# Performance work log

Hardware: AMD Instinct MI355X
Metric: run time of the kernel (lower is better)

The kernel has to match this reference:

```python
import jax, jax.numpy as jnp
import numpy as np

# Multi-scale deformable attention encoder (Mask2Former pixel decoder transformer)
SHAPES = ((64, 64), (32, 32), (16, 16))  # (H, W) per level, strides 8/16/32 of 512x512
HEADS, POINTS, DM = 8, 4, 256
HD = DM // HEADS
NLVL = len(SHAPES)
NLAYERS = 6
STARTS = np.concatenate([[0], np.cumsum([h * w for h, w in SHAPES])])


def layer_norm(x, g, b, eps=1e-5):
    m = x.mean(-1, keepdims=True)
    v = ((x - m) ** 2).mean(-1, keepdims=True)
    return (x - m) * jax.lax.rsqrt(v + eps) * g + b


def ref_points(B, dtype):
    # valid_ratios == 1 (masks are all-False in the module)
    pts = []
    for H, W in SHAPES:
        ys = (jnp.arange(H, dtype=dtype) + 0.5) / H
        xs = (jnp.arange(W, dtype=dtype) + 0.5) / W
        gy, gx = jnp.meshgrid(ys, xs, indexing='ij')
        pts.append(jnp.stack([gx.reshape(-1), gy.reshape(-1)], -1))
    ref = jnp.concatenate(pts, 0)  # [Q,2]
    return jnp.broadcast_to(ref[None, :, None, :], (B, ref.shape[0], NLVL, 2))


def bilinear(value, loc, H, W):
    # grid_sample(align_corners=False, padding_mode='zeros')
    # value: [B,heads,H*W,d]; loc: [B,Q,heads,P,2] normalized to [0,1]
    x = loc[..., 0] * W - 0.5
    y = loc[..., 1] * H - 0.5
    x0f = jnp.floor(x); y0f = jnp.floor(y)
    lx = x - x0f; ly = y - y0f
    x0 = x0f.astype(jnp.int32); y0 = y0f.astype(jnp.int32)
    out = 0.
    for dx, dy, w in ((0, 0, (1 - lx) * (1 - ly)), (1, 0, lx * (1 - ly)),
                      (0, 1, (1 - lx) * ly), (1, 1, lx * ly)):
        xi = x0 + dx; yi = y0 + dy
        valid = (xi >= 0) & (xi < W) & (yi >= 0) & (yi < H)
        idx = jnp.clip(yi, 0, H - 1) * W + jnp.clip(xi, 0, W - 1)  # [B,Q,heads,P]
        idx_t = jnp.transpose(idx, (0, 2, 1, 3))  # [B,heads,Q,P]
        Bq, hq, Qq, Pq = idx_t.shape
        g = jnp.take_along_axis(value, idx_t.reshape(Bq, hq, Qq * Pq, 1), axis=2)
        g = g.reshape(Bq, hq, Qq, Pq, HD)
        wv = (w * valid).transpose(0, 2, 1, 3)[..., None]  # [B,heads,Q,P,1]
        out = out + g * wv
    return out  # [B,heads,Q,P,d]


def msda(query, src, ref, p):
    off_w, off_b, aw_w, aw_b, val_w, val_b, out_w, out_b = p
    B, Q, _ = query.shape
    value = (src @ val_w.T + val_b).reshape(B, Q, HEADS, HD).transpose(0, 2, 1, 3)  # [B,h,Q,d]
    off = (query @ off_w.T + off_b).reshape(B, Q, HEADS, NLVL, POINTS, 2)
    aw = (query @ aw_w.T + aw_b).reshape(B, Q, HEADS, NLVL * POINTS)
    aw = jax.nn.softmax(aw, -1).reshape(B, Q, HEADS, NLVL, POINTS)
    norm = jnp.array([[W, H] for H, W in SHAPES], dtype=query.dtype)  # [L,2] as (W,H)
    loc = ref[:, :, None, :, None, :] + off / norm[None, None, None, :, None, :]
    samp = []
    for l, (H, W) in enumerate(SHAPES):
        v = value[:, :, STARTS[l]:STARTS[l + 1], :]
        samp.append(bilinear(v, loc[:, :, :, l], H, W))  # [B,h,Q,P,d]
    samp = jnp.stack(samp, 3)  # [B,h,Q,L,P,d]
    w = aw.transpose(0, 2, 1, 3, 4)[..., None]  # [B,h,Q,L,P,1]
    o = (samp * w).sum((3, 4)).transpose(0, 2, 1, 3).reshape(B, Q, DM)
    return o @ out_w.T + out_b


def reference(src0, src1, src2, pos0, pos1, pos2, level_embed,
              off_w, off_b, aw_w, aw_b, val_w, val_b, out_w, out_b,
              ln1_g, ln1_b, ffn1_w, ffn1_b, ffn2_w, ffn2_b, ln2_g, ln2_b):
    srcs, poss = [src0, src1, src2], [pos0, pos1, pos2]
    B = src0.shape[0]
    xs, ps = [], []
    for l, (s, pe) in enumerate(zip(srcs, poss)):
        b, c, h, w = s.shape
        xs.append(s.reshape(b, c, h * w).transpose(0, 2, 1))
        ps.append(pe.reshape(b, c, h * w).transpose(0, 2, 1) + level_embed[l])
    x = jnp.concatenate(xs, 1)    # [B,Q,C]
    pos = jnp.concatenate(ps, 1)  # [B,Q,C]
    ref = ref_points(B, x.dtype)
    for i in range(NLAYERS):
        q = x + pos
        attn = msda(q, x, ref, (off_w[i], off_b[i], aw_w[i], aw_b[i],
                                val_w[i], val_b[i], out_w[i], out_b[i]))
        x = layer_norm(x + attn, ln1_g[i], ln1_b[i])
        h = jax.nn.relu(x @ ffn1_w[i].T + ffn1_b[i])
        x = layer_norm(x + h @ ffn2_w[i].T + ffn2_b[i], ln2_g[i], ln2_b[i])
    return x  # memory [B,Q,C]


def setup_inputs() -> dict:
    key = jax.random.key(0)
    ks = jax.random.split(key, 16)
    s = 0.02
    inp = {}
    inp['src0'] = jax.random.normal(ks[0], (4, 256, 64, 64), jnp.float32)
    inp['src1'] = jax.random.normal(ks[1], (4, 256, 32, 32), jnp.float32)
    inp['src2'] = jax.random.normal(ks[2], (4, 256, 16, 16), jnp.float32)
    inp['pos0'] = jax.random.normal(ks[3], (4, 256, 64, 64), jnp.float32)
    inp['pos1'] = jax.random.normal(ks[4], (4, 256, 32, 32), jnp.float32)
    inp['pos2'] = jax.random.normal(ks[5], (4, 256, 16, 16), jnp.float32)
    inp['level_embed'] = jax.random.normal(ks[6], (3, 256), jnp.float32)
    inp['off_w'] = jax.random.normal(ks[7], (6, 192, 256), jnp.float32) * s
    inp['off_b'] = jnp.zeros((6, 192), jnp.float32)
    inp['aw_w'] = jax.random.normal(ks[8], (6, 96, 256), jnp.float32) * s
    inp['aw_b'] = jnp.zeros((6, 96), jnp.float32)
    inp['val_w'] = jax.random.normal(ks[9], (6, 256, 256), jnp.float32) * s
    inp['val_b'] = jnp.zeros((6, 256), jnp.float32)
    inp['out_w'] = jax.random.normal(ks[10], (6, 256, 256), jnp.float32) * s
    inp['out_b'] = jnp.zeros((6, 256), jnp.float32)
    inp['ln1_g'] = jnp.ones((6, 256), jnp.float32)
    inp['ln1_b'] = jnp.zeros((6, 256), jnp.float32)
    inp['ffn1_w'] = jax.random.normal(ks[11], (6, 1024, 256), jnp.float32) * s
    inp['ffn1_b'] = jnp.zeros((6, 1024), jnp.float32)
    inp['ffn2_w'] = jax.random.normal(ks[12], (6, 256, 1024), jnp.float32) * s
    inp['ffn2_b'] = jnp.zeros((6, 256), jnp.float32)
    inp['ln2_g'] = jnp.ones((6, 256), jnp.float32)
    inp['ln2_b'] = jnp.zeros((6, 256), jnp.float32)
    return inp
```

## Files before the change

kernel.cpp:

```cpp
#include <hip/hip_runtime.h>
#include <hip/hip_bf16.h>
#include <math.h>

#define BB 4
#define QTOT 5376
#define DMM 256
#define NHEADS 8
#define HDIM 32
#define NPTS 4
#define NLVLS 3
#define BQ (BB*QTOT)
#define NOA 288

typedef short bf16x8 __attribute__((ext_vector_type(8)));
typedef unsigned short u16x8 __attribute__((ext_vector_type(8)));
typedef float f32x4  __attribute__((ext_vector_type(4)));

__device__ __forceinline__ unsigned short f2b(float f) {
  unsigned int u = __float_as_uint(f);
  unsigned int r = (u + 0x7FFFu + ((u >> 16) & 1u)) >> 16;
  return (unsigned short)r;
}
__device__ __forceinline__ float b2f(unsigned short u) {
  return __uint_as_float(((unsigned int)u) << 16);
}
__device__ __forceinline__ ushort4 f2b4(float4 v) {
  ushort4 o; o.x = f2b(v.x); o.y = f2b(v.y); o.z = f2b(v.z); o.w = f2b(v.w);
  return o;
}

__device__ __forceinline__ void gload16(const void* g, void* l) {
  __builtin_amdgcn_global_load_lds(
      (const __attribute__((address_space(1))) void*)g,
      (__attribute__((address_space(3))) void*)l, 16, 0, 0);
}

__global__ __launch_bounds__(256) void transpose2(
    const float* __restrict__ src, const float* __restrict__ pos,
    const float* __restrict__ emb, float* __restrict__ x,
    unsigned short* __restrict__ pos16, int HW, int qstart)
{
  __shared__ float ts[32][33];
  __shared__ float tp[32][33];
  int hw0 = blockIdx.x * 32, c0 = blockIdx.y * 32, b = blockIdx.z;
  int tx = threadIdx.x, ty = threadIdx.y;
  const float* s = src + ((size_t)b * DMM + c0) * HW + hw0;
  const float* p = pos + ((size_t)b * DMM + c0) * HW + hw0;
#pragma unroll
  for (int j = 0; j < 4; j++) {
    ts[ty * 4 + j][tx] = s[(size_t)(ty * 4 + j) * HW + tx];
    tp[ty * 4 + j][tx] = p[(size_t)(ty * 4 + j) * HW + tx];
  }
  __syncthreads();
  float e = emb[c0 + tx];
  size_t base = ((size_t)b * QTOT + qstart + hw0) * DMM + c0;
#pragma unroll
  for (int j = 0; j < 4; j++) {
    x[base + (size_t)(ty * 4 + j) * DMM + tx] = ts[tx][ty * 4 + j];
    pos16[base + (size_t)(ty * 4 + j) * DMM + tx] = f2b(tp[tx][ty * 4 + j] + e);
  }
}

__global__ __launch_bounds__(256) void conv_b(
    const float* __restrict__ s, unsigned short* __restrict__ d, int n4)
{
  int i = blockIdx.x * 256 + threadIdx.x;
  if (i >= n4) return;
  ((ushort4*)d)[i] = f2b4(((const float4*)s)[i]);
}

__global__ __launch_bounds__(256) void pack_oa(
    const float* __restrict__ offw, const float* __restrict__ aww,
    unsigned short* __restrict__ dst)
{
  int i = blockIdx.x * 256 + threadIdx.x;
  if (i >= 6 * NOA * 64) return;
  int c4 = i & 63;
  int row = (i >> 6) % NOA;
  int l = i / (NOA * 64);
  const float* src = (row < 192)
      ? offw + ((size_t)l * 192 + row) * 256
      : aww  + ((size_t)l * 96 + (row - 192)) * 256;
  float4 v = ((const float4*)src)[c4];
  ((ushort4*)dst)[i] = f2b4(v);
}

__global__ __launch_bounds__(256) void pack_oa_bias(
    const float* __restrict__ offb, const float* __restrict__ awb,
    float* __restrict__ dst)
{
  int i = blockIdx.x * 256 + threadIdx.x;
  if (i >= 6 * NOA) return;
  int row = i % NOA, l = i / NOA;
  dst[i] = (row < 192) ? offb[l * 192 + row] : awb[l * 96 + (row - 192)];
}

__global__ __launch_bounds__(256) void prep(
    const float* __restrict__ x, const unsigned short* __restrict__ pos16,
    unsigned short* __restrict__ xb, unsigned short* __restrict__ qb, int n4)
{
  int i = blockIdx.x * 256 + threadIdx.x;
  if (i >= n4) return;
  float4 a = ((const float4*)x)[i];
  ushort4 p = ((const ushort4*)pos16)[i];
  ((ushort4*)xb)[i] = f2b4(a);
  ushort4 q;
  q.x = f2b(a.x + b2f(p.x)); q.y = f2b(a.y + b2f(p.y));
  q.z = f2b(a.z + b2f(p.z)); q.w = f2b(a.w + b2f(p.w));
  ((ushort4*)qb)[i] = q;
}

__device__ __forceinline__ void gemm_tile_body(
    const unsigned short* __restrict__ A, const unsigned short* __restrict__ W,
    int m0, int n0, int K,
    unsigned short (*As)[32], unsigned short (*Ws)[32], f32x4 acc[4][4])
{
  int tid = threadIdx.x;
  int wave = tid >> 6, lane = tid & 63;
  int lr = lane & 15;
  int lkr = ((lane >> 4) ^ (lane & 3)) * 8;
  int wrr = (wave >> 1) * 64;
  int wcc = (wave & 1) * 64;

  int srow = lane >> 2;
  int schunk = ((lane & 3) ^ (srow & 3)) * 8;
  const unsigned short* Ag = A + (size_t)(m0 + wave * 32 + srow) * K + schunk;
  const unsigned short* Wg = W + (size_t)(n0 + wave * 32 + srow) * K + schunk;

#define STAGE_BF(k0, buf)                                                      \
  { int bo = (buf) * 128 + wave * 32;                                          \
    gload16(Ag + (k0), &As[bo][0]);                                            \
    gload16(Ag + (size_t)16 * K + (k0), &As[bo + 16][0]);                      \
    gload16(Wg + (k0), &Ws[bo][0]);                                            \
    gload16(Wg + (size_t)16 * K + (k0), &Ws[bo + 16][0]); }

  STAGE_BF(0, 0);
  __syncthreads();
  int cur = 0;
  for (int k0 = 0; k0 < K; k0 += 32) {
    if (k0 + 32 < K) STAGE_BF(k0 + 32, cur ^ 1);
    int bo = cur * 128;
    bf16x8 af[4], bfv[4];
#pragma unroll
    for (int m = 0; m < 4; m++)
      af[m] = *(const bf16x8*)&As[bo + wrr + m * 16 + lr][lkr];
#pragma unroll
    for (int n = 0; n < 4; n++)
      bfv[n] = *(const bf16x8*)&Ws[bo + wcc + n * 16 + lr][lkr];
#pragma unroll
    for (int m = 0; m < 4; m++)
#pragma unroll
      for (int n = 0; n < 4; n++)
        acc[m][n] = __builtin_amdgcn_mfma_f32_16x16x32_bf16(af[m], bfv[n], acc[m][n], 0, 0, 0);
    __syncthreads();
    cur ^= 1;
  }
#undef STAGE_BF
}

__device__ __forceinline__ void gemm_epilogue(
    const float* __restrict__ bias, void* __restrict__ Cout,
    int m0, int n0, int N, int relu, int bfout, f32x4 acc[4][4])
{
  int tid = threadIdx.x;
  int wave = tid >> 6, lane = tid & 63;
  int lr = lane & 15;
  int wrr = (wave >> 1) * 64;
  int wcc = (wave & 1) * 64;
  float* C32 = (float*)Cout;
  unsigned short* C16 = (unsigned short*)Cout;
#pragma unroll
  for (int n = 0; n < 4; n++) {
    int col = n0 + wcc + n * 16 + lr;
    if (col >= N) continue;
    float bv = bias[col];
#pragma unroll
    for (int m = 0; m < 4; m++) {
      int row0 = m0 + wrr + m * 16 + (lane >> 4) * 4;
#pragma unroll
      for (int j = 0; j < 4; j++) {
        float v = acc[m][n][j] + bv;
        if (relu) v = fmaxf(v, 0.0f);
        if (bfout) C16[(size_t)(row0 + j) * N + col] = f2b(v);
        else       C32[(size_t)(row0 + j) * N + col] = v;
      }
    }
  }
}

__global__ __launch_bounds__(256) void gemm_bf(
    const unsigned short* __restrict__ A, const unsigned short* __restrict__ W,
    const float* __restrict__ bias, void* __restrict__ Cout,
    int M, int N, int K, int flags)
{
  __shared__ unsigned short As[256][32];
  __shared__ unsigned short Ws[256][32];
  f32x4 acc[4][4] = {};
  int m0 = blockIdx.x * 128, n0 = blockIdx.y * 128;
  gemm_tile_body(A, W, m0, n0, K, As, Ws, acc);
  gemm_epilogue(bias, Cout, m0, n0, N, flags & 1, flags & 2, acc);
}

__global__ __launch_bounds__(256) void gemm_valoa(
    const unsigned short* __restrict__ xb, const unsigned short* __restrict__ qb,
    const unsigned short* __restrict__ vW, const unsigned short* __restrict__ oaW,
    const float* __restrict__ vBias, const float* __restrict__ oaBias,
    unsigned short* __restrict__ valb16, unsigned short* __restrict__ offaw16)
{
  __shared__ unsigned short As[256][32];
  __shared__ unsigned short Ws[256][32];
  f32x4 acc[4][4] = {};
  int m0 = blockIdx.x * 128;
  int by = blockIdx.y;
  const int K = 256;
  if (by < 2) {
    int n0 = by * 128;
    gemm_tile_body(xb, vW, m0, n0, K, As, Ws, acc);
    gemm_epilogue(vBias, valb16, m0, n0, 256, 0, 2, acc);
  } else {
    int n0 = (by - 2) * 128;
    gemm_tile_body(qb, oaW, m0, n0, K, As, Ws, acc);
    gemm_epilogue(oaBias, offaw16, m0, n0, NOA, 0, 2, acc);
  }
}

__global__ __launch_bounds__(512) void gemm_ln(
    const unsigned short* __restrict__ A, const unsigned short* __restrict__ W,
    const float* __restrict__ bias, const float* __restrict__ g,
    const float* __restrict__ beta, float* __restrict__ x,
    unsigned short* __restrict__ xb, const unsigned short* __restrict__ pos16,
    unsigned short* __restrict__ qb, int K)
{
  __shared__ unsigned short As[64][32];
  __shared__ unsigned short Ws[512][32];

  int m0 = blockIdx.x * 32;
  int tid = threadIdx.x;
  int wave = tid >> 6, lane = tid & 63;
  int lr = lane & 15;
  int lkr = ((lane >> 4) ^ (lane & 3)) * 8;
  int srow = lane >> 2;
  int schunk = ((lane & 3) ^ (srow & 3)) * 8;

  const unsigned short* Ag = A + (size_t)(m0 + (wave & 1) * 16 + srow) * K + schunk;
  const unsigned short* Wg = W + (size_t)(wave * 32 + srow) * K + schunk;

#define STAGE_LN(k0, buf)                                                      \
  { if (wave < 2) gload16(Ag + (k0), &As[(buf) * 32 + wave * 16][0]);          \
    gload16(Wg + (k0),                  &Ws[(buf) * 256 + wave * 32][0]);      \
    gload16(Wg + (size_t)16 * K + (k0), &Ws[(buf) * 256 + wave * 32 + 16][0]); }

  f32x4 acc[2][2] = {};

  STAGE_LN(0, 0);
  __syncthreads();
  int cur = 0;
  for (int k0 = 0; k0 < K; k0 += 32) {
    if (k0 + 32 < K) STAGE_LN(k0 + 32, cur ^ 1);
    bf16x8 af[2], bfv[2];
#pragma unroll
    for (int m = 0; m < 2; m++)
      af[m] = *(const bf16x8*)&As[cur * 32 + m * 16 + lr][lkr];
#pragma unroll
    for (int n = 0; n < 2; n++)
      bfv[n] = *(const bf16x8*)&Ws[cur * 256 + wave * 32 + n * 16 + lr][lkr];
#pragma unroll
    for (int m = 0; m < 2; m++)
#pragma unroll
      for (int n = 0; n < 2; n++)
        acc[m][n] = __builtin_amdgcn_mfma_f32_16x16x32_bf16(af[m], bfv[n], acc[m][n], 0, 0, 0);
    __syncthreads();
    cur ^= 1;
  }
#undef STAGE_LN

#pragma unroll
  for (int n = 0; n < 2; n++) {
    int col = wave * 32 + n * 16 + lr;
    float bv = bias[col];
#pragma unroll
    for (int m = 0; m < 2; m++) {
      int grow = m0 + m * 16 + (lane >> 4) * 4;
#pragma unroll
      for (int j = 0; j < 4; j++)
        acc[m][n][j] += bv + x[(size_t)(grow + j) * DMM + col];
    }
  }

  float2* red = (float2*)&As[0][0];
#pragma unroll
  for (int m = 0; m < 2; m++) {
#pragma unroll
    for (int j = 0; j < 4; j++) {
      float s  = acc[m][0][j] + acc[m][1][j];
      float s2 = acc[m][0][j] * acc[m][0][j] + acc[m][1][j] * acc[m][1][j];
#pragma unroll
      for (int o = 1; o < 16; o <<= 1) {
        s  += __shfl_xor(s,  o, 64);
        s2 += __shfl_xor(s2, o, 64);
      }
      if (lr == 0)
        red[(m * 16 + (lane >> 4) * 4 + j) * 8 + wave] = make_float2(s, s2);
    }
  }
  __syncthreads();

#pragma unroll
  for (int m = 0; m < 2; m++) {
#pragma unroll
    for (int j = 0; j < 4; j++) {
      int rl = m * 16 + (lane >> 4) * 4 + j;
      float ts = 0.f, ts2 = 0.f;
#pragma unroll
      for (int wv = 0; wv < 8; wv++) {
        float2 r = red[rl * 8 + wv];
        ts += r.x; ts2 += r.y;
      }
      float mean = ts * (1.0f / DMM);
      float var  = ts2 * (1.0f / DMM) - mean * mean;
      float sc = rsqrtf(var + 1e-5f);
      int grow = m0 + rl;
#pragma unroll
      for (int n = 0; n < 2; n++) {
        int col = wave * 32 + n * 16 + lr;
        float o = (acc[m][n][j] - mean) * sc * g[col] + beta[col];
        size_t idx = (size_t)grow * DMM + col;
        x[idx]  = o;
        xb[idx] = f2b(o);
        if (qb) qb[idx] = f2b(o + b2f(pos16[idx]));
      }
    }
  }
}

__global__ __launch_bounds__(256) void msda_sample(
    const unsigned short* __restrict__ value, const unsigned short* __restrict__ offaw16,
    unsigned short* __restrict__ attn16)
{
  __shared__ float saw[8][96];
  __shared__ float smx[64], sinv[64];
  __shared__ float swgt[768 * 4];
  __shared__ int   sofs[768 * 4];

  int tid = threadIdx.x;
  int qi = tid >> 5, t32 = tid & 31;
  int h = t32 >> 2, dg = t32 & 3;
  int bq0 = blockIdx.x * 8;
  int bq = bq0 + qi;
  int b = bq / QTOT;

  for (int i = t32; i < 96; i += 32)
    saw[qi][i] = b2f(offaw16[(size_t)bq * NOA + 192 + i]);
  __syncthreads();

  if (tid < 64) {
    int q2 = tid >> 3, h2 = tid & 7;
    float mx = -1e30f;
#pragma unroll
    for (int t = 0; t < 12; t++) mx = fmaxf(mx, saw[q2][h2 * 12 + t]);
    float den = 0.f;
#pragma unroll
    for (int t = 0; t < 12; t++) den += __expf(saw[q2][h2 * 12 + t] - mx);
    smx[tid] = mx;
    sinv[tid] = 1.0f / den;
  }
  __syncthreads();

  for (int s = tid; s < 768; s += 256) {
    int p = s >> 6;
    int qh = s & 63;
    int q2 = qh >> 3, h2 = qh & 7;
    int l = p >> 2;
    int Wl = 64 >> l;
    int st = (l == 0) ? 0 : ((l == 1) ? 4096 : 5120);

    int q = (bq0 + q2) % QTOT;
    int qq, Wq;
    if (q < 4096)      { qq = q;        Wq = 64; }
    else if (q < 5120) { qq = q - 4096; Wq = 32; }
    else               { qq = q - 5120; Wq = 16; }
    float refx = ((qq % Wq) + 0.5f) / Wq;
    float refy = ((qq / Wq) + 0.5f) / Wq;

    int oi = ((h2 * NLVLS + l) * NPTS + (p & 3)) * 2;
    ushort2 ob = *(const ushort2*)&offaw16[(size_t)(bq0 + q2) * NOA + oi];
    float offx = b2f(ob.x), offy = b2f(ob.y);
    float invW = 1.0f / (float)Wl;
    float xf = (refx + offx * invW) * Wl - 0.5f;
    float yf = (refy + offy * invW) * Wl - 0.5f;
    float x0f = floorf(xf), y0f = floorf(yf);
    float fx = xf - x0f, fy = yf - y0f;
    int x0 = (int)x0f, y0 = (int)y0f;

    float aw = __expf(saw[q2][h2 * 12 + p] - smx[qh]) * sinv[qh];
    float w00 = (1.f - fx) * (1.f - fy) * aw;
    float w10 = fx * (1.f - fy) * aw;
    float w01 = (1.f - fx) * fy * aw;
    float w11 = fx * fy * aw;

    bool xv0 = (x0 >= 0) & (x0 < Wl);
    bool xv1 = (x0 + 1 >= 0) & (x0 + 1 < Wl);
    bool yv0 = (y0 >= 0) & (y0 < Wl);
    bool yv1 = (y0 + 1 >= 0) & (y0 + 1 < Wl);

    int base = s * 4;
    swgt[base + 0] = (xv0 & yv0) ? w00 : 0.f;
    swgt[base + 1] = (xv1 & yv0) ? w10 : 0.f;
    swgt[base + 2] = (xv0 & yv1) ? w01 : 0.f;
    swgt[base + 3] = (xv1 & yv1) ? w11 : 0.f;
    sofs[base + 0] = (xv0 & yv0) ? (st + y0 * Wl + x0) * (DMM * 2) : 0;
    sofs[base + 1] = (xv1 & yv0) ? (st + y0 * Wl + x0 + 1) * (DMM * 2) : 0;
    sofs[base + 2] = (xv0 & yv1) ? (st + (y0 + 1) * Wl + x0) * (DMM * 2) : 0;
    sofs[base + 3] = (xv1 & yv1) ? (st + (y0 + 1) * Wl + x0 + 1) * (DMM * 2) : 0;
  }
  __syncthreads();

  float a8[8];
#pragma unroll
  for (int k = 0; k < 8; k++) a8[k] = 0.f;
  const char* vbase = (const char*)(value + (size_t)b * QTOT * DMM + h * HDIM + dg * 8);
#pragma unroll
  for (int p = 0; p < 12; p++) {
    int s3 = (p * 64 + qi * 8 + h) * 4;
    float4 w = *(const float4*)&swgt[s3];
    int4  of = *(const int4*)&sofs[s3];
    u16x8 g0 = *(const u16x8*)(vbase + of.x);
    u16x8 g1 = *(const u16x8*)(vbase + of.y);
    u16x8 g2 = *(const u16x8*)(vbase + of.z);
    u16x8 g3 = *(const u16x8*)(vbase + of.w);
#pragma unroll
    for (int k = 0; k < 8; k++)
      a8[k] += w.x * b2f((unsigned short)g0[k]) + w.y * b2f((unsigned short)g1[k])
             + w.z * b2f((unsigned short)g2[k]) + w.w * b2f((unsigned short)g3[k]);
  }
  u16x8 o;
#pragma unroll
  for (int k = 0; k < 8; k++) o[k] = f2b(a8[k]);
  *(u16x8*)(attn16 + (size_t)bq * DMM + h * HDIM + dg * 8) = o;
}

extern "C" void kernel_launch(void* const* d_in, const int* in_sizes, int n_in,
                              void* d_out, int out_size, void* d_ws, size_t ws_size,
                              hipStream_t stream)
{
  const float* src[3] = {(const float*)d_in[0], (const float*)d_in[1], (const float*)d_in[2]};
  const float* pin[3] = {(const float*)d_in[3], (const float*)d_in[4], (const float*)d_in[5]};
  const float* lvl_emb = (const float*)d_in[6];
  const float* off_w = (const float*)d_in[7];
  const float* off_b = (const float*)d_in[8];
  const float* aw_w  = (const float*)d_in[9];
  const float* aw_b  = (const float*)d_in[10];
  const float* val_w = (const float*)d_in[11];
  const float* val_b = (const float*)d_in[12];
  const float* out_w = (const float*)d_in[13];
  const float* out_b = (const float*)d_in[14];
  const float* ln1_g = (const float*)d_in[15];
  const float* ln1_b = (const float*)d_in[16];
  const float* ffn1_w = (const float*)d_in[17];
  const float* ffn1_b = (const float*)d_in[18];
  const float* ffn2_w = (const float*)d_in[19];
  const float* ffn2_b = (const float*)d_in[20];
  const float* ln2_g = (const float*)d_in[21];
  const float* ln2_b = (const float*)d_in[22];

  float* x = (float*)d_out;

  char* wsp = (char*)d_ws;
  unsigned short* offaw16 = (unsigned short*)wsp; wsp += (size_t)BQ * NOA * 2;
  unsigned short* valb16  = (unsigned short*)wsp; wsp += (size_t)BQ * 256 * 2;
  unsigned short* attnb   = (unsigned short*)wsp; wsp += (size_t)BQ * 256 * 2;
  unsigned short* hb = offaw16;
  wsp += (size_t)10 * 1024 * 1024;
  unsigned short* pos16 = (unsigned short*)wsp; wsp += (size_t)BQ * 256 * 2;
  unsigned short* xb = (unsigned short*)wsp; wsp += (size_t)BQ * 256 * 2;
  unsigned short* qb = (unsigned short*)wsp; wsp += (size_t)BQ * 256 * 2;

  unsigned short* vWb  = (unsigned short*)wsp; wsp += (size_t)6 * 256 * 256 * 2;
  unsigned short* oaWb = (unsigned short*)wsp; wsp += (size_t)6 * NOA * 256 * 2;
  unsigned short* uWb  = (unsigned short*)wsp; wsp += (size_t)6 * 256 * 256 * 2;
  unsigned short* f1Wb = (unsigned short*)wsp; wsp += (size_t)6 * 1024 * 256 * 2;
  unsigned short* f2Wb = (unsigned short*)wsp; wsp += (size_t)6 * 256 * 1024 * 2;
  float* oaBias = (float*)wsp; wsp += (size_t)6 * NOA * 4;
  wsp += 65536;

  conv_b<<<(6 * 65536 / 4 + 255) / 256, 256, 0, stream>>>(val_w, vWb, 6 * 65536 / 4);
  conv_b<<<(6 * 65536 / 4 + 255) / 256, 256, 0, stream>>>(out_w, uWb, 6 * 65536 / 4);
  conv_b<<<(6 * 262144 / 4 + 255) / 256, 256, 0, stream>>>(ffn1_w, f1Wb, 6 * 262144 / 4);
  conv_b<<<(6 * 262144 / 4 + 255) / 256, 256, 0, stream>>>(ffn2_w, f2Wb, 6 * 262144 / 4);
  pack_oa<<<(6 * NOA * 64 + 255) / 256, 256, 0, stream>>>(off_w, aw_w, oaWb);
  pack_oa_bias<<<(6 * NOA + 255) / 256, 256, 0, stream>>>(off_b, aw_b, oaBias);

  const int HWs[3] = {4096, 1024, 256};
  const int starts[3] = {0, 4096, 5120};
  for (int l = 0; l < 3; l++) {
    dim3 g(HWs[l] / 32, DMM / 32, BB), blk(32, 8);
    transpose2<<<g, blk, 0, stream>>>(src[l], pin[l], lvl_emb + l * 256,
                                      x, pos16, HWs[l], starts[l]);
  }
  prep<<<(BQ * 256 / 4 + 255) / 256, 256, 0, stream>>>(x, pos16, xb, qb, BQ * 256 / 4);

  for (int i = 0; i < 6; i++) {
    gemm_valoa<<<dim3(BQ / 128, 5), 256, 0, stream>>>(
        xb, qb, vWb + (size_t)i * 65536, oaWb + (size_t)i * NOA * 256,
        val_b + i * 256, oaBias + i * NOA, valb16, offaw16);
    msda_sample<<<BQ / 8, 256, 0, stream>>>(valb16, offaw16, attnb);
    gemm_ln<<<BQ / 32, 512, 0, stream>>>(attnb, uWb + (size_t)i * 65536,
        out_b + i * 256, ln1_g + i * 256, ln1_b + i * 256, x, xb,
        nullptr, nullptr, 256);
    gemm_bf<<<dim3(BQ / 128, 8), 256, 0, stream>>>(xb, f1Wb + (size_t)i * 262144,
        ffn1_b + i * 1024, hb, BQ, 1024, 256, 1 | 2);
    gemm_ln<<<BQ / 32, 512, 0, stream>>>(hb, f2Wb + (size_t)i * 262144,
        ffn2_b + i * 256, ln2_g + i * 256, ln2_b + i * 256, x, xb,
        pos16, qb, 1024);
  }
}
```

Before: 921.9 us.

## Fuse FFN1, ReLU and FFN2 with LayerNorm into one kernel

Replaces the separate FFN1 GEMM, which wrote a 1024-wide bf16 hidden tensor to global memory, and the FFN2+LayerNorm GEMM with a single kernel. Each 32-row block keeps its input tile in LDS, computes the hidden activations in 256-column chunks into LDS, and immediately accumulates them into the FFN2 output before the residual add and LayerNorm. This removes the hidden-tensor round trip and one launch per layer. In exchange, each block streams the full W1 and W2 weights (small M tile, so weight reuse drops), runs with many __syncthreads, and uses a single-buffered weight pipeline.

```diff
diff --git a/kernel.cpp b/kernel.cpp
--- a/kernel.cpp
+++ b/kernel.cpp
@@ -186,19 +186,6 @@
       }
     }
   }
-}
-
-__global__ __launch_bounds__(256) void gemm_bf(
-    const unsigned short* __restrict__ A, const unsigned short* __restrict__ W,
-    const float* __restrict__ bias, void* __restrict__ Cout,
-    int M, int N, int K, int flags)
-{
-  __shared__ unsigned short As[256][32];
-  __shared__ unsigned short Ws[256][32];
-  f32x4 acc[4][4] = {};
-  int m0 = blockIdx.x * 128, n0 = blockIdx.y * 128;
-  gemm_tile_body(A, W, m0, n0, K, As, Ws, acc);
-  gemm_epilogue(bias, Cout, m0, n0, N, flags & 1, flags & 2, acc);
 }
 
 __global__ __launch_bounds__(256) void gemm_valoa(
@@ -328,6 +315,160 @@
         x[idx]  = o;
         xb[idx] = f2b(o);
         if (qb) qb[idx] = f2b(o + b2f(pos16[idx]));
+      }
+    }
+  }
+}
+
+__global__ __launch_bounds__(512) void ffn_ln(
+    const unsigned short* __restrict__ xbin, const unsigned short* __restrict__ W1,
+    const float* __restrict__ b1, const unsigned short* __restrict__ W2,
+    const float* __restrict__ b2, const float* __restrict__ g,
+    const float* __restrict__ beta, float* __restrict__ x,
+    unsigned short* __restrict__ xb, const unsigned short* __restrict__ pos16,
+    unsigned short* __restrict__ qb)
+{
+  __shared__ unsigned short AxbF[32 * 256];
+  __shared__ unsigned short Hc[32][264];
+  __shared__ unsigned short Ws[256][40];
+  __shared__ float2 red[32 * 8];
+
+  int m0 = blockIdx.x * 32;
+  int tid = threadIdx.x;
+  int wave = tid >> 6, lane = tid & 63;
+  int lr = lane & 15;
+  int p4 = lane >> 4;
+
+  int wrow = tid >> 2, wchk = tid & 3;
+
+#define WSRC(s2, fr)                                                            \
+  ( (((s2) >> 3) & 1) == 0                                                      \
+    ? W1 + ((size_t)(((s2) >> 4) * 256 + (fr))) * 256 + ((s2) & 7) * 32 + wchk * 8 \
+    : W2 + ((size_t)(fr)) * 1024 + ((s2) >> 4) * 256 + ((s2) & 7) * 32 + wchk * 8 )
+
+#pragma unroll
+  for (int j = 0; j < 2; j++) {
+    int f2 = j * 512 + tid;
+    int arow = f2 >> 5, achk = f2 & 31;
+    gload16(xbin + (size_t)(m0 + arow) * 256 + ((achk ^ arow) & 31) * 8,
+            &AxbF[(size_t)(j * 512 + wave * 64) * 8]);
+  }
+  {
+    uint4 wa = *(const uint4*)WSRC(0, wrow);
+    uint4 wb = *(const uint4*)WSRC(0, wrow + 128);
+    *(u16x8*)&Ws[wrow][wchk * 8] = *(u16x8*)&wa;
+    *(u16x8*)&Ws[wrow + 128][wchk * 8] = *(u16x8*)&wb;
+  }
+  __syncthreads();
+
+  f32x4 ao[2][2] = {};
+
+#define FSTEP(S, ACC, AF0, AF1)                                                \
+  { uint4 wa, wb; const int sn = (S) + 1;                                      \
+    if (sn < 64) {                                                             \
+      wa = *(const uint4*)WSRC(sn, wrow);                                      \
+      wb = *(const uint4*)WSRC(sn, wrow + 128);                                \
+    }                                                                          \
+    bf16x8 af0 = (AF0), af1 = (AF1);                                           \
+    bf16x8 bf0 = *(const bf16x8*)&Ws[wave * 32 + lr][p4 * 8];                  \
+    bf16x8 bf1 = *(const bf16x8*)&Ws[wave * 32 + 16 + lr][p4 * 8];             \
+    ACC[0][0] = __builtin_amdgcn_mfma_f32_16x16x32_bf16(af0, bf0, ACC[0][0], 0, 0, 0); \
+    ACC[0][1] = __builtin_amdgcn_mfma_f32_16x16x32_bf16(af0, bf1, ACC[0][1], 0, 0, 0); \
+    ACC[1][0] = __builtin_amdgcn_mfma_f32_16x16x32_bf16(af1, bf0, ACC[1][0], 0, 0, 0); \
+    ACC[1][1] = __builtin_amdgcn_mfma_f32_16x16x32_bf16(af1, bf1, ACC[1][1], 0, 0, 0); \
+    __syncthreads();                                                           \
+    if (sn < 64) {                                                             \
+      *(u16x8*)&Ws[wrow][wchk * 8] = *(u16x8*)&wa;                             \
+      *(u16x8*)&Ws[wrow + 128][wchk * 8] = *(u16x8*)&wb;                       \
+    } }
+
+#pragma unroll
+  for (int ch = 0; ch < 4; ++ch) {
+    f32x4 ah[2][2] = {};
+#pragma unroll
+    for (int w = 0; w < 8; ++w) {
+      FSTEP(ch * 16 + w, ah,
+        (*(const bf16x8*)&AxbF[(size_t)lr * 256 + (((w * 4 + p4) ^ lr) & 31) * 8]),
+        (*(const bf16x8*)&AxbF[(size_t)(16 + lr) * 256 + (((w * 4 + p4) ^ (16 + lr)) & 31) * 8]));
+      if (w == 7) {
+#pragma unroll
+        for (int n2 = 0; n2 < 2; n2++) {
+          float bb = b1[ch * 256 + wave * 32 + n2 * 16 + lr];
+#pragma unroll
+          for (int m2 = 0; m2 < 2; m2++)
+#pragma unroll
+            for (int j = 0; j < 4; j++) {
+              float v = ah[m2][n2][j] + bb;
+              Hc[m2 * 16 + p4 * 4 + j][wave * 32 + n2 * 16 + lr] = f2b(fmaxf(v, 0.f));
+            }
+        }
+      }
+      __syncthreads();
+    }
+#pragma unroll
+    for (int w = 0; w < 8; ++w) {
+      FSTEP(ch * 16 + 8 + w, ao,
+        (*(const bf16x8*)&Hc[lr][w * 32 + p4 * 8]),
+        (*(const bf16x8*)&Hc[16 + lr][w * 32 + p4 * 8]));
+      if (ch * 16 + 8 + w < 63) __syncthreads();
+    }
+  }
+#undef FSTEP
+#undef WSRC
+
+#pragma unroll
+  for (int n = 0; n < 2; n++) {
+    int col = wave * 32 + n * 16 + lr;
+    float bv = b2[col];
+#pragma unroll
+    for (int m = 0; m < 2; m++) {
+      int grow = m0 + m * 16 + p4 * 4;
+#pragma unroll
+      for (int j = 0; j < 4; j++)
+        ao[m][n][j] += bv + x[(size_t)(grow + j) * DMM + col];
+    }
+  }
+
+#pragma unroll
+  for (int m = 0; m < 2; m++) {
+#pragma unroll
+    for (int j = 0; j < 4; j++) {
+      float s  = ao[m][0][j] + ao[m][1][j];
+      float s2 = ao[m][0][j] * ao[m][0][j] + ao[m][1][j] * ao[m][1][j];
+#pragma unroll
+      for (int o = 1; o < 16; o <<= 1) {
+        s  += __shfl_xor(s,  o, 64);
+        s2 += __shfl_xor(s2, o, 64);
+      }
+      if (lr == 0)
+        red[(m * 16 + p4 * 4 + j) * 8 + wave] = make_float2(s, s2);
+    }
+  }
+  __syncthreads();
+
+#pragma unroll
+  for (int m = 0; m < 2; m++) {
+#pragma unroll
+    for (int j = 0; j < 4; j++) {
+      int rl = m * 16 + p4 * 4 + j;
+      float ts = 0.f, ts2 = 0.f;
+#pragma unroll
+      for (int wv = 0; wv < 8; wv++) {
+        float2 r = red[rl * 8 + wv];
+        ts += r.x; ts2 += r.y;
+      }
+      float mean = ts * (1.0f / DMM);
+      float var  = ts2 * (1.0f / DMM) - mean * mean;
+      float sc = rsqrtf(var + 1e-5f);
+      int grow = m0 + rl;
+#pragma unroll
+      for (int n = 0; n < 2; n++) {
+        int col = wave * 32 + n * 16 + lr;
+        float o = (ao[m][n][j] - mean) * sc * g[col] + beta[col];
+        size_t idx = (size_t)grow * DMM + col;
+        x[idx]  = o;
+        xb[idx] = f2b(o);
+        qb[idx] = f2b(o + b2f(pos16[idx]));
       }
     }
   }
@@ -469,8 +610,6 @@
   unsigned short* offaw16 = (unsigned short*)wsp; wsp += (size_t)BQ * NOA * 2;
   unsigned short* valb16  = (unsigned short*)wsp; wsp += (size_t)BQ * 256 * 2;
   unsigned short* attnb   = (unsigned short*)wsp; wsp += (size_t)BQ * 256 * 2;
-  unsigned short* hb = offaw16;
-  wsp += (size_t)10 * 1024 * 1024;
   unsigned short* pos16 = (unsigned short*)wsp; wsp += (size_t)BQ * 256 * 2;
   unsigned short* xb = (unsigned short*)wsp; wsp += (size_t)BQ * 256 * 2;
   unsigned short* qb = (unsigned short*)wsp; wsp += (size_t)BQ * 256 * 2;
@@ -507,10 +646,8 @@
     gemm_ln<<<BQ / 32, 512, 0, stream>>>(attnb, uWb + (size_t)i * 65536,
         out_b + i * 256, ln1_g + i * 256, ln1_b + i * 256, x, xb,
         nullptr, nullptr, 256);
-    gemm_bf<<<dim3(BQ / 128, 8), 256, 0, stream>>>(xb, f1Wb + (size_t)i * 262144,
-        ffn1_b + i * 1024, hb, BQ, 1024, 256, 1 | 2);
-    gemm_ln<<<BQ / 32, 512, 0, stream>>>(hb, f2Wb + (size_t)i * 262144,
-        ffn2_b + i * 256, ln2_g + i * 256, ln2_b + i * 256, x, xb,
-        pos16, qb, 1024);
-  }
-}
+    ffn_ln<<<BQ / 32, 512, 0, stream>>>(xb, f1Wb + (size_t)i * 262144,
+        ffn1_b + i * 1024, f2Wb + (size_t)i * 262144, ffn2_b + i * 256,
+        ln2_g + i * 256, ln2_b + i * 256, x, xb, pos16, qb);
+  }
+}
```

Result: slower. 942.7 us (+2.3%).
